# Performance work log

Measured on AMD Instinct MI355X. Metric: run time of the kernel, lower is better.

The kernel has to match this reference:

```python
import jax, jax.numpy as jnp
import numpy as np

N = 1_000_000   # number of scattered source rows
M = 50_000      # number of attention keys / segments
D = 128         # values_dim == keys_dim


def setup_inputs() -> dict:
    key = jax.random.key(0)
    k1, k2, k3, k4, k5 = jax.random.split(key, 5)
    scattered_values = jax.random.normal(k1, (N, D), dtype=jnp.float32)
    indices = jax.random.randint(k2, (N,), 0, M, dtype=jnp.int64)
    attn_keys = jax.random.normal(k3, (M, D), dtype=jnp.float32)
    W = jax.random.normal(k4, (D, D), dtype=jnp.float32) * (1.0 / np.sqrt(D))
    b = jax.random.normal(k5, (D,), dtype=jnp.float32) * 0.01
    return {"scattered_values": scattered_values, "indices": indices,
            "attn_keys": attn_keys, "W": W, "b": b}


def reference(scattered_values, indices, attn_keys, W, b):
    num_segments = attn_keys.shape[0]
    # linear key projection: [M, D]
    keys_proj = attn_keys @ W.T + b
    # gather projected keys per source row: [N, D]
    gathered = keys_proj[indices]
    # per-row dot-product score: [N]
    probs = jnp.sum(scattered_values * gathered, axis=1)
    # segment-wise (scatter) softmax over rows sharing the same index
    seg_max = jax.ops.segment_max(probs, indices, num_segments=num_segments)
    ex = jnp.exp(probs - seg_max[indices])
    seg_sum = jax.ops.segment_sum(ex, indices, num_segments=num_segments)
    scattered_scores = ex / seg_sum[indices]
    # scatter-sum of score-weighted values: [M, D]
    attn_applied = jax.ops.segment_sum(
        scattered_values * scattered_scores[:, None], indices,
        num_segments=num_segments)
    return scattered_scores, attn_applied
```

## Files before the change

### kernel.cpp

```cpp
#include <hip/hip_runtime.h>
#include <float.h>

#define D 128

__global__ __launch_bounds__(256) void k_keys_proj(
    const float* __restrict__ attn_keys, const float* __restrict__ W,
    const float* __restrict__ b, float* __restrict__ keys_proj, int M) {
  __shared__ float sKey[32][D + 1];
  __shared__ float sWt[32][D + 1];
  const int tid = threadIdx.x;
  const int tc = tid & 31;
  const int tr = tid >> 5;
  const int row0 = blockIdx.x * 32;

  for (int e = tid; e < 32 * D; e += 256) {
    int r = e >> 7, k = e & (D - 1);
    int row = row0 + r;
    sKey[r][k] = (row < M) ? attn_keys[(size_t)row * D + k] : 0.0f;
  }

  float acc[4][4];
#pragma unroll
  for (int i = 0; i < 4; ++i)
#pragma unroll
    for (int c = 0; c < 4; ++c) acc[i][c] = 0.0f;

  for (int kc = 0; kc < D; kc += 32) {
    __syncthreads();
    for (int e = tid; e < 32 * D; e += 256) {
      int k = e & 31, j = e >> 5;
      sWt[k][j] = W[(size_t)j * D + kc + k];
    }
    __syncthreads();
#pragma unroll 8
    for (int kk = 0; kk < 32; ++kk) {
      float kv[4], wv[4];
#pragma unroll
      for (int i = 0; i < 4; ++i) kv[i] = sKey[4 * tr + i][kc + kk];
#pragma unroll
      for (int c = 0; c < 4; ++c) wv[c] = sWt[kk][4 * tc + c];
#pragma unroll
      for (int i = 0; i < 4; ++i)
#pragma unroll
        for (int c = 0; c < 4; ++c) acc[i][c] += kv[i] * wv[c];
    }
  }

#pragma unroll
  for (int i = 0; i < 4; ++i) {
    int row = row0 + 4 * tr + i;
    if (row < M) {
#pragma unroll
      for (int c = 0; c < 4; ++c) {
        int j = 4 * tc + c;
        keys_proj[(size_t)row * D + j] = acc[i][c] + b[j];
      }
    }
  }
}

__global__ __launch_bounds__(256) void k_count(
    const int* __restrict__ indices, int* __restrict__ counts, int N) {
  int i = blockIdx.x * blockDim.x + threadIdx.x;
  const int stride = gridDim.x * blockDim.x;
  for (; i < N; i += stride) atomicAdd(counts + indices[i], 1);
}

__global__ __launch_bounds__(256) void k_offsets(
    const int* __restrict__ counts, int* __restrict__ fillpos,
    int* __restrict__ cursor, int M) {
  int m = blockIdx.x * blockDim.x + threadIdx.x;
  if (m < M) fillpos[m] = atomicAdd(cursor, counts[m]);
}

__global__ __launch_bounds__(256) void k_fill(
    const int* __restrict__ indices, int* __restrict__ fillpos,
    int* __restrict__ rowids, int N) {
  int i = blockIdx.x * blockDim.x + threadIdx.x;
  const int stride = gridDim.x * blockDim.x;
  for (; i < N; i += stride) {
    int p = atomicAdd(fillpos + indices[i], 1);
    rowids[p] = i;
  }
}

__global__ __launch_bounds__(256) void k_segment(
    const float* __restrict__ values, const int* __restrict__ rowids,
    const int* __restrict__ counts, const int* __restrict__ fillpos,
    const float* __restrict__ keys_proj, float* __restrict__ raw_scores,
    float* __restrict__ seg_m, float* __restrict__ seg_l,
    float* __restrict__ attn_out, int M) {
  const int lane = threadIdx.x & 63;
  const int wid = (int)((blockIdx.x * blockDim.x + threadIdx.x) >> 6);
  const int nw = (int)((gridDim.x * blockDim.x) >> 6);

  for (int m = wid; m < M; m += nw) {
    const int cnt = counts[m];
    const int start = fillpos[m] - cnt;
    const float2 k = ((const float2*)(keys_proj + (size_t)m * D))[lane];

    float run_m = -FLT_MAX, run_l = 0.0f;
    float2 acc = {0.0f, 0.0f};

    int i_next = 0;
    float2 v_next = {0.0f, 0.0f};
    if (cnt > 0) {
      i_next = rowids[start];
      v_next = ((const float2*)(values + (size_t)i_next * D))[lane];
    }

    for (int r = 0; r < cnt; ++r) {
      const int i = i_next;
      const float2 v = v_next;
      if (r + 1 < cnt) {
        i_next = rowids[start + r + 1];
        v_next = ((const float2*)(values + (size_t)i_next * D))[lane];
      }
      float s = v.x * k.x + v.y * k.y;
#pragma unroll
      for (int off = 32; off > 0; off >>= 1) s += __shfl_xor(s, off, 64);
      if (lane == 0) raw_scores[i] = s;
      const float mn = fmaxf(run_m, s);
      const float alpha = __expf(run_m - mn);
      const float p = __expf(s - mn);
      run_l = run_l * alpha + p;
      acc.x = acc.x * alpha + p * v.x;
      acc.y = acc.y * alpha + p * v.y;
      run_m = mn;
    }

    const float inv = (cnt > 0) ? 1.0f / run_l : 0.0f;
    float2 out = {acc.x * inv, acc.y * inv};
    ((float2*)(attn_out + (size_t)m * D))[lane] = out;
    if (lane == 0) {
      seg_m[m] = run_m;
      seg_l[m] = run_l;
    }
  }
}

__global__ __launch_bounds__(256) void k_scores(
    const int* __restrict__ indices, const float* __restrict__ seg_m,
    const float* __restrict__ seg_l, float* __restrict__ scores, int N) {
  int i = blockIdx.x * blockDim.x + threadIdx.x;
  const int stride = gridDim.x * blockDim.x;
  for (; i < N; i += stride) {
    const int m = indices[i];
    scores[i] = __expf(scores[i] - seg_m[m]) / seg_l[m];
  }
}

extern "C" void kernel_launch(void* const* d_in, const int* in_sizes, int n_in,
                              void* d_out, int out_size, void* d_ws, size_t ws_size,
                              hipStream_t stream) {
  const float* values = (const float*)d_in[0];
  const int* indices = (const int*)d_in[1];
  const float* attn_keys = (const float*)d_in[2];
  const float* W = (const float*)d_in[3];
  const float* b = (const float*)d_in[4];
  const int N = in_sizes[0] / D;
  const int M = in_sizes[2] / D;

  float* keys_proj = (float*)d_ws;
  int* counts = (int*)(keys_proj + (size_t)M * D);
  int* fillpos = counts + M;
  float* seg_mv = (float*)(fillpos + M);
  float* seg_lv = seg_mv + M;
  int* cursor = (int*)(seg_lv + M);
  int* rowids = cursor + 64;

  float* scores = (float*)d_out;
  float* attn_out = scores + N;

  hipMemsetAsync(counts, 0, (size_t)M * sizeof(int), stream);
  hipMemsetAsync(cursor, 0, 64 * sizeof(int), stream);

  k_keys_proj<<<(M + 31) / 32, 256, 0, stream>>>(attn_keys, W, b, keys_proj, M);
  k_count<<<1024, 256, 0, stream>>>(indices, counts, N);
  k_offsets<<<(M + 255) / 256, 256, 0, stream>>>(counts, fillpos, cursor, M);
  k_fill<<<1024, 256, 0, stream>>>(indices, fillpos, rowids, N);
  k_segment<<<2048, 256, 0, stream>>>(values, rowids, counts, fillpos, keys_proj,
                                      scores, seg_mv, seg_lv, attn_out, M);
  k_scores<<<1024, 256, 0, stream>>>(indices, seg_mv, seg_lv, scores, N);
}
```

Before: 997.5 us.

## Fuse score normalization into segment kernel and process four rows per wave

The segment kernel now splits each wave into four 16-lane groups that each handle a different row of the segment. Each lane loads float4 pairs, and the per-row online-softmax updates are combined with rescaling factors. Raw scores are kept in shared memory, spilling to a workspace buffer past 512 per segment, so the final normalized scores are written inside the same kernel. This removes the separate k_scores pass and its indices/seg_m/seg_l gathers. The count and fill kernels also read indices as int4. The trade-offs are more shuffle and exp work per row group, and scattered score writes through rowids.

Measured after the change: 892.9 us. 10.5% less time.

```diff
diff --git a/kernel.cpp b/kernel.cpp
--- a/kernel.cpp
+++ b/kernel.cpp
@@ -2,6 +2,7 @@
 #include <float.h>
 
 #define D 128
+#define CAP 512
 
 __global__ __launch_bounds__(256) void k_keys_proj(
     const float* __restrict__ attn_keys, const float* __restrict__ W,
@@ -63,7 +64,16 @@
     const int* __restrict__ indices, int* __restrict__ counts, int N) {
   int i = blockIdx.x * blockDim.x + threadIdx.x;
   const int stride = gridDim.x * blockDim.x;
-  for (; i < N; i += stride) atomicAdd(counts + indices[i], 1);
+  const int n4 = N >> 2;
+  const int4* idx4 = (const int4*)indices;
+  for (int j = i; j < n4; j += stride) {
+    int4 v = idx4[j];
+    atomicAdd(counts + v.x, 1);
+    atomicAdd(counts + v.y, 1);
+    atomicAdd(counts + v.z, 1);
+    atomicAdd(counts + v.w, 1);
+  }
+  for (int j = (n4 << 2) + i; j < N; j += stride) atomicAdd(counts + indices[j], 1);
 }
 
 __global__ __launch_bounds__(256) void k_offsets(
@@ -78,75 +88,129 @@
     int* __restrict__ rowids, int N) {
   int i = blockIdx.x * blockDim.x + threadIdx.x;
   const int stride = gridDim.x * blockDim.x;
-  for (; i < N; i += stride) {
-    int p = atomicAdd(fillpos + indices[i], 1);
-    rowids[p] = i;
-  }
+  const int n4 = N >> 2;
+  const int4* idx4 = (const int4*)indices;
+  for (int j = i; j < n4; j += stride) {
+    int4 v = idx4[j];
+    int base = 4 * j;
+    rowids[atomicAdd(fillpos + v.x, 1)] = base;
+    rowids[atomicAdd(fillpos + v.y, 1)] = base + 1;
+    rowids[atomicAdd(fillpos + v.z, 1)] = base + 2;
+    rowids[atomicAdd(fillpos + v.w, 1)] = base + 3;
+  }
+  for (int j = (n4 << 2) + i; j < N; j += stride)
+    rowids[atomicAdd(fillpos + indices[j], 1)] = j;
 }
 
 __global__ __launch_bounds__(256) void k_segment(
     const float* __restrict__ values, const int* __restrict__ rowids,
     const int* __restrict__ counts, const int* __restrict__ fillpos,
-    const float* __restrict__ keys_proj, float* __restrict__ raw_scores,
-    float* __restrict__ seg_m, float* __restrict__ seg_l,
-    float* __restrict__ attn_out, int M) {
+    const float* __restrict__ keys_proj, float* __restrict__ raw_ovf,
+    float* __restrict__ scores, float* __restrict__ attn_out, int M) {
+  __shared__ float sS[4][CAP];
   const int lane = threadIdx.x & 63;
-  const int wid = (int)((blockIdx.x * blockDim.x + threadIdx.x) >> 6);
-  const int nw = (int)((gridDim.x * blockDim.x) >> 6);
-
-  for (int m = wid; m < M; m += nw) {
-    const int cnt = counts[m];
-    const int start = fillpos[m] - cnt;
-    const float2 k = ((const float2*)(keys_proj + (size_t)m * D))[lane];
-
-    float run_m = -FLT_MAX, run_l = 0.0f;
-    float2 acc = {0.0f, 0.0f};
-
-    int i_next = 0;
-    float2 v_next = {0.0f, 0.0f};
-    if (cnt > 0) {
-      i_next = rowids[start];
-      v_next = ((const float2*)(values + (size_t)i_next * D))[lane];
-    }
-
-    for (int r = 0; r < cnt; ++r) {
-      const int i = i_next;
-      const float2 v = v_next;
-      if (r + 1 < cnt) {
-        i_next = rowids[start + r + 1];
-        v_next = ((const float2*)(values + (size_t)i_next * D))[lane];
-      }
-      float s = v.x * k.x + v.y * k.y;
-#pragma unroll
-      for (int off = 32; off > 0; off >>= 1) s += __shfl_xor(s, off, 64);
-      if (lane == 0) raw_scores[i] = s;
-      const float mn = fmaxf(run_m, s);
-      const float alpha = __expf(run_m - mn);
-      const float p = __expf(s - mn);
-      run_l = run_l * alpha + p;
-      acc.x = acc.x * alpha + p * v.x;
-      acc.y = acc.y * alpha + p * v.y;
-      run_m = mn;
-    }
-
-    const float inv = (cnt > 0) ? 1.0f / run_l : 0.0f;
-    float2 out = {acc.x * inv, acc.y * inv};
-    ((float2*)(attn_out + (size_t)m * D))[lane] = out;
+  const int wv = threadIdx.x >> 6;
+  const int m = blockIdx.x * 4 + wv;
+  if (m >= M) return;
+  const int g = lane >> 4;
+  const int t = lane & 15;
+
+  const int cnt = counts[m];
+  const int start = fillpos[m] - cnt;
+
+  const float4* kp = (const float4*)(keys_proj + (size_t)m * D);
+  const float4 k1 = kp[2 * t], k2 = kp[2 * t + 1];
+  const float4* vr = (const float4*)values;
+
+  float run_m = -FLT_MAX, run_l = 0.0f;
+  float4 accA = {0, 0, 0, 0}, accB = {0, 0, 0, 0};
+
+  float4 a = {0, 0, 0, 0}, b = {0, 0, 0, 0};
+  if (cnt > 0) {
+    int id = rowids[start + min(g, cnt - 1)];
+    a = vr[(size_t)id * 32 + 2 * t];
+    b = vr[(size_t)id * 32 + 2 * t + 1];
+  }
+
+  for (int gb = 0; gb < cnt; gb += 4) {
+    const float4 ca = a, cb = b;
+    if (gb + 4 < cnt) {
+      int nid = rowids[start + min(gb + 4 + g, cnt - 1)];
+      a = vr[(size_t)nid * 32 + 2 * t];
+      b = vr[(size_t)nid * 32 + 2 * t + 1];
+    }
+    float s = ca.x * k1.x + ca.y * k1.y + ca.z * k1.z + ca.w * k1.w +
+              cb.x * k2.x + cb.y * k2.y + cb.z * k2.z + cb.w * k2.w;
+    s += __shfl_xor(s, 1, 64);
+    s += __shfl_xor(s, 2, 64);
+    s += __shfl_xor(s, 4, 64);
+    s += __shfl_xor(s, 8, 64);
+    const float s0 = __shfl(s, 0, 64);
+    const float s1 = __shfl(s, 16, 64);
+    const float s2 = __shfl(s, 32, 64);
+    const float s3 = __shfl(s, 48, 64);
+
+    float al0, al1, al2, al3, p0, p1, p2, p3;
+#define STEP(sj, actj, alj, pj)                                   \
+    {                                                             \
+      float ss = (actj) ? (sj) : -FLT_MAX;                        \
+      float mn = fmaxf(run_m, ss);                                \
+      alj = __expf(run_m - mn);                                   \
+      pj = (actj) ? __expf(ss - mn) : 0.0f;                       \
+      run_l = run_l * alj + pj;                                   \
+      run_m = mn;                                                 \
+    }
+    STEP(s0, true, al0, p0);
+    STEP(s1, gb + 1 < cnt, al1, p1);
+    STEP(s2, gb + 2 < cnt, al2, p2);
+    STEP(s3, gb + 3 < cnt, al3, p3);
+#undef STEP
+    const float f3 = 1.0f;
+    const float f2 = al3;
+    const float f1 = al3 * al2;
+    const float f0 = f1 * al1;
+    const float scale = f0 * al0;
+    const float w = (g == 0) ? p0 * f0 : (g == 1) ? p1 * f1
+                  : (g == 2) ? p2 * f2 : p3 * f3;
+    accA.x = accA.x * scale + ca.x * w;
+    accA.y = accA.y * scale + ca.y * w;
+    accA.z = accA.z * scale + ca.z * w;
+    accA.w = accA.w * scale + ca.w * w;
+    accB.x = accB.x * scale + cb.x * w;
+    accB.y = accB.y * scale + cb.y * w;
+    accB.z = accB.z * scale + cb.z * w;
+    accB.w = accB.w * scale + cb.w * w;
+
     if (lane == 0) {
-      seg_m[m] = run_m;
-      seg_l[m] = run_l;
-    }
-  }
-}
-
-__global__ __launch_bounds__(256) void k_scores(
-    const int* __restrict__ indices, const float* __restrict__ seg_m,
-    const float* __restrict__ seg_l, float* __restrict__ scores, int N) {
-  int i = blockIdx.x * blockDim.x + threadIdx.x;
-  const int stride = gridDim.x * blockDim.x;
-  for (; i < N; i += stride) {
-    const int m = indices[i];
-    scores[i] = __expf(scores[i] - seg_m[m]) / seg_l[m];
+      int r = gb;
+      if (r < cnt) { if (r < CAP) sS[wv][r] = s0; else raw_ovf[start + r] = s0; }
+      r = gb + 1;
+      if (r < cnt) { if (r < CAP) sS[wv][r] = s1; else raw_ovf[start + r] = s1; }
+      r = gb + 2;
+      if (r < cnt) { if (r < CAP) sS[wv][r] = s2; else raw_ovf[start + r] = s2; }
+      r = gb + 3;
+      if (r < cnt) { if (r < CAP) sS[wv][r] = s3; else raw_ovf[start + r] = s3; }
+    }
+  }
+
+#define RED(x) x += __shfl_xor(x, 16, 64); x += __shfl_xor(x, 32, 64)
+  RED(accA.x); RED(accA.y); RED(accA.z); RED(accA.w);
+  RED(accB.x); RED(accB.y); RED(accB.z); RED(accB.w);
+#undef RED
+
+  const float invl = (run_l > 0.0f) ? 1.0f / run_l : 0.0f;
+  if (g == 0) {
+    float4* op = (float4*)(attn_out + (size_t)m * D);
+    float4 oA = {accA.x * invl, accA.y * invl, accA.z * invl, accA.w * invl};
+    float4 oB = {accB.x * invl, accB.y * invl, accB.z * invl, accB.w * invl};
+    op[2 * t] = oA;
+    op[2 * t + 1] = oB;
+  }
+
+  for (int r = lane; r < cnt; r += 64) {
+    const float s = (r < CAP) ? sS[wv][r] : raw_ovf[start + r];
+    const int i = rowids[start + r];
+    scores[i] = __expf(s - run_m) * invl;
   }
 }
 
@@ -164,10 +228,9 @@
   float* keys_proj = (float*)d_ws;
   int* counts = (int*)(keys_proj + (size_t)M * D);
   int* fillpos = counts + M;
-  float* seg_mv = (float*)(fillpos + M);
-  float* seg_lv = seg_mv + M;
-  int* cursor = (int*)(seg_lv + M);
+  int* cursor = fillpos + M;
   int* rowids = cursor + 64;
+  float* raw_ovf = (float*)(rowids + N);
 
   float* scores = (float*)d_out;
   float* attn_out = scores + N;
@@ -179,7 +242,6 @@
   k_count<<<1024, 256, 0, stream>>>(indices, counts, N);
   k_offsets<<<(M + 255) / 256, 256, 0, stream>>>(counts, fillpos, cursor, M);
   k_fill<<<1024, 256, 0, stream>>>(indices, fillpos, rowids, N);
-  k_segment<<<2048, 256, 0, stream>>>(values, rowids, counts, fillpos, keys_proj,
-                                      scores, seg_mv, seg_lv, attn_out, M);
-  k_scores<<<1024, 256, 0, stream>>>(indices, seg_mv, seg_lv, scores, N);
-}
+  k_segment<<<(M + 3) / 4, 256, 0, stream>>>(values, rowids, counts, fillpos,
+                                             keys_proj, raw_ovf, scores, attn_out, M);
+}
```
